# Kernel optimization log

Measured on AMD Instinct MI355X. Metric: run time of the kernel, lower is better.

The kernel has to match this reference:

```python
import jax, jax.numpy as jnp
import numpy as np
from jax import lax

DIM, HEADS, HIDDEN = 384, 6, 1536
B, D, H, W = 2, 14, 14, 14
LN_EPS = 1e-5


def setup_inputs() -> dict:
    key = jax.random.key(0)
    ks = jax.random.split(key, 8)
    s = 0.02
    return {
        "x": jax.random.normal(ks[0], (B, DIM, D, H, W), jnp.float32),
        "conv_w": jax.random.normal(ks[1], (DIM, 1, 3, 3, 3), jnp.float32) * s,
        "conv_b": jnp.zeros((DIM,), jnp.float32),
        "ln1_w": jnp.ones((DIM,), jnp.float32),
        "ln1_b": jnp.zeros((DIM,), jnp.float32),
        "qkv_w": jax.random.normal(ks[2], (3 * DIM, DIM), jnp.float32) * s,
        "proj_w": jax.random.normal(ks[3], (DIM, DIM), jnp.float32) * s,
        "proj_b": jnp.zeros((DIM,), jnp.float32),
        "ln2_w": jnp.ones((DIM,), jnp.float32),
        "ln2_b": jnp.zeros((DIM,), jnp.float32),
        "fc1_w": jax.random.normal(ks[4], (HIDDEN, DIM), jnp.float32) * s,
        "fc1_b": jnp.zeros((HIDDEN,), jnp.float32),
        "fc2_w": jax.random.normal(ks[5], (DIM, HIDDEN), jnp.float32) * s,
        "fc2_b": jnp.zeros((DIM,), jnp.float32),
    }


def _layernorm(x, w, b):
    mu = jnp.mean(x, axis=-1, keepdims=True)
    var = jnp.var(x, axis=-1, keepdims=True)
    return (x - mu) * lax.rsqrt(var + LN_EPS) * w + b


def reference(x, conv_w, conv_b, ln1_w, ln1_b, qkv_w, proj_w, proj_b,
              ln2_w, ln2_b, fc1_w, fc1_b, fc2_w, fc2_b):
    Bn, C = x.shape[0], x.shape[1]
    Dd, Hh, Ww = x.shape[2], x.shape[3], x.shape[4]
    # depthwise conv3d positional embedding (groups=dim), padding=1
    pos = lax.conv_general_dilated(
        x, conv_w, window_strides=(1, 1, 1), padding="SAME",
        feature_group_count=C,
        dimension_numbers=("NCDHW", "OIDHW", "NCDHW"))
    x = x + pos + conv_b[None, :, None, None, None] * 0 + conv_b[None, :, None, None, None]
    # fix: bias belongs to conv output only once
    x = x - conv_b[None, :, None, None, None]
    N = Dd * Hh * Ww
    t = x.reshape(Bn, C, N).transpose(0, 2, 1)  # [B, N, C]

    # attention
    hd = C // HEADS
    scale = hd ** -0.5
    tn = _layernorm(t, ln1_w, ln1_b)
    qkv = tn @ qkv_w.T  # [B, N, 3C]
    qkv = qkv.reshape(Bn, N, 3, HEADS, hd).transpose(2, 0, 3, 1, 4)
    q, k, v = qkv[0], qkv[1], qkv[2]  # [B, H, N, hd]
    attn = jax.nn.softmax(jnp.einsum("bhnd,bhmd->bhnm", q, k) * scale, axis=-1)
    o = jnp.einsum("bhnm,bhmd->bhnd", attn, v)
    o = o.transpose(0, 2, 1, 3).reshape(Bn, N, C)
    t = t + o @ proj_w.T + proj_b

    # MLP (exact GELU, matching torch nn.GELU default)
    tn2 = _layernorm(t, ln2_w, ln2_b)
    h = jax.nn.gelu(tn2 @ fc1_w.T + fc1_b, approximate=False)
    t = t + h @ fc2_w.T + fc2_b

    return t.transpose(0, 2, 1).reshape(Bn, C, Dd, Hh, Ww)
```

## Files before the change

### kernel.cpp

```cpp
#include <hip/hip_runtime.h>
#include <hip/hip_bf16.h>
#include <math.h>

#define DIM 384
#define HEADS 6
#define HIDDEN 1536
#define NTOK 2744
#define BATCH 2
#define MTOT (BATCH * NTOK)
#define KSPLIT 4
#define NQT 22
#define CEXP 0.18033688f

typedef __bf16 bf16x8 __attribute__((ext_vector_type(8)));
typedef __bf16 bf16x4 __attribute__((ext_vector_type(4)));
typedef float  f32x4  __attribute__((ext_vector_type(4)));

#define F_GELU  1
#define F_RESID 2
#define F_BF16  4
#define F_QKV   8
#define F_TRANS 16

__device__ __forceinline__ void gll16(const void* g, void* l) {
    __builtin_amdgcn_global_load_lds(
        (const __attribute__((address_space(1))) unsigned int*)g,
        (__attribute__((address_space(3))) unsigned int*)l, 16, 0, 0);
}

__global__ void k_conv(const float* __restrict__ x, const float* __restrict__ cw,
                       float* __restrict__ t,
                       const float* __restrict__ w0, const float* __restrict__ w1,
                       const float* __restrict__ w2, const float* __restrict__ w3,
                       __bf16* o0, __bf16* o1, __bf16* o2, __bf16* o3) {
    int bid = blockIdx.x;
    if (bid >= 528) {
        int i = (bid - 528) * 256 + threadIdx.x;
        const float* s; __bf16* d; int off;
        if (i < 110592)      { s = w0; d = o0; off = i; }
        else if (i < 147456) { s = w1; d = o1; off = i - 110592; }
        else if (i < 294912) { s = w2; d = o2; off = i - 147456; }
        else                 { s = w3; d = o3; off = i - 294912; }
        float4 v = ((const float4*)s)[off];
        bf16x4 bb = { (__bf16)v.x, (__bf16)v.y, (__bf16)v.z, (__bf16)v.w };
        *(bf16x4*)(d + (size_t)off * 4) = bb;
        return;
    }
    int nb = bid % 11, rest = bid / 11;
    int cb = rest % 24, b = rest / 24;
    int c0 = cb * 16;
    int n = nb * 256 + threadIdx.x;
    if (n >= NTOK) return;
    int d = n / 196, r = n % 196, h = r / 14, w = r % 14;
    const float* xb = x + ((size_t)b * DIM + c0) * NTOK;
    float acc[16];
    #pragma unroll
    for (int c = 0; c < 16; c++) acc[c] = xb[(size_t)c * NTOK + n];
    #pragma unroll
    for (int kd = 0; kd < 3; kd++) {
        int dd = d + kd - 1;
        if (dd < 0 || dd >= 14) continue;
        #pragma unroll
        for (int kh = 0; kh < 3; kh++) {
            int hh = h + kh - 1;
            if (hh < 0 || hh >= 14) continue;
            #pragma unroll
            for (int kw = 0; kw < 3; kw++) {
                int ww = w + kw - 1;
                if (ww < 0 || ww >= 14) continue;
                int np = (dd * 14 + hh) * 14 + ww;
                int tap = kd * 9 + kh * 3 + kw;
                #pragma unroll
                for (int c = 0; c < 16; c++)
                    acc[c] = fmaf(cw[(c0 + c) * 27 + tap], xb[(size_t)c * NTOK + np], acc[c]);
            }
        }
    }
    float* tp = t + (size_t)(b * NTOK + n) * DIM + c0;
    #pragma unroll
    for (int c = 0; c < 16; c += 4) {
        float4 v = { acc[c], acc[c + 1], acc[c + 2], acc[c + 3] };
        *(float4*)(tp + c) = v;
    }
}

__device__ __forceinline__ void ln_body(const float* __restrict__ in,
                                        __bf16* __restrict__ out,
                                        const float* __restrict__ w,
                                        const float* __restrict__ b) {
    int wid = threadIdx.x >> 6, lane = threadIdx.x & 63;
    int token = blockIdx.x * 4 + wid;
    const float* row = in + (size_t)token * DIM;
    float v[6], s = 0.f, s2 = 0.f;
    #pragma unroll
    for (int i = 0; i < 6; i++) {
        v[i] = row[lane + 64 * i];
        s += v[i]; s2 += v[i] * v[i];
    }
    #pragma unroll
    for (int m = 1; m < 64; m <<= 1) { s += __shfl_xor(s, m); s2 += __shfl_xor(s2, m); }
    float mu = s * (1.f / DIM);
    float rstd = rsqrtf(s2 * (1.f / DIM) - mu * mu + 1e-5f);
    __bf16* orow = out + (size_t)token * DIM;
    #pragma unroll
    for (int i = 0; i < 6; i++) {
        int c = lane + 64 * i;
        orow[c] = (__bf16)((v[i] - mu) * rstd * w[c] + b[c]);
    }
}
__global__ void k_ln1(const float* in, __bf16* out, const float* w, const float* b) {
    ln_body(in, out, w, b);
}
__global__ void k_ln2(const float* in, __bf16* out, const float* w, const float* b) {
    ln_body(in, out, w, b);
}

__device__ __forceinline__ void gemm12864_body(
    const __bf16* __restrict__ A, const __bf16* __restrict__ B,
    const float* __restrict__ bias, void* __restrict__ out,
    __bf16* __restrict__ vt_out, int M, int N, int K, int flags) {
    __shared__ __bf16 As[128][64];
    __shared__ __bf16 Bs[64][64];
    int tid = threadIdx.x, lane = tid & 63, wid = tid >> 6;
    int quad = lane >> 4, l16 = lane & 15;
    int wm = wid & 1, wn = wid >> 1;
    int m0 = blockIdx.y * 128, n0 = blockIdx.x * 64;
    int x7 = l16 & 7;

    auto stage = [&](int k0) {
        #pragma unroll
        for (int i = 0; i < 4; i++) {
            int c = i * 256 + tid;
            int row = c >> 3, cc = (c & 7) ^ (row & 7);
            int gm = m0 + row; if (gm > M - 1) gm = M - 1;
            gll16(A + (size_t)gm * K + k0 + cc * 8, &As[0][0] + (size_t)c * 8);
        }
        #pragma unroll
        for (int i = 0; i < 2; i++) {
            int c = i * 256 + tid;
            int row = c >> 3, cc = (c & 7) ^ (row & 7);
            gll16(B + (size_t)(n0 + row) * K + k0 + cc * 8, &Bs[0][0] + (size_t)c * 8);
        }
    };

    f32x4 acc[4][2] = {};
    int nk = K >> 6;
    for (int ki = 0; ki < nk; ki++) {
        if (ki) __syncthreads();
        stage(ki << 6);
        __syncthreads();
        #pragma unroll
        for (int s = 0; s < 2; s++) {
            bf16x8 a[4], b[2];
            #pragma unroll
            for (int i = 0; i < 4; i++)
                a[i] = *(bf16x8*)&As[wm * 64 + i * 16 + l16][(((s * 4 + quad) ^ x7)) * 8];
            #pragma unroll
            for (int j = 0; j < 2; j++)
                b[j] = *(bf16x8*)&Bs[wn * 32 + j * 16 + l16][(((s * 4 + quad) ^ x7)) * 8];
            #pragma unroll
            for (int i = 0; i < 4; i++)
                #pragma unroll
                for (int j = 0; j < 2; j++)
                    acc[i][j] = __builtin_amdgcn_mfma_f32_16x16x32_bf16(a[i], b[j], acc[i][j], 0, 0, 0);
        }
    }

    int colb = n0 + wn * 32;
    #pragma unroll
    for (int j = 0; j < 2; j++) {
        int col = colb + j * 16 + l16;
        float bv = bias ? bias[col] : 0.f;
        #pragma unroll
        for (int i = 0; i < 4; i++) {
            int row0 = m0 + wm * 64 + i * 16 + quad * 4;
            if (row0 >= M) continue;
            float v4[4];
            #pragma unroll
            for (int r = 0; r < 4; r++) {
                float v = acc[i][j][r] + bv;
                if (flags & F_GELU) v = 0.5f * v * (1.f + erff(v * 0.70710678f));
                if ((flags & F_QKV) && col < 384) v *= CEXP;
                v4[r] = v;
            }
            if ((flags & F_QKV) && col >= 768) {
                int b2 = row0 / NTOK, n2 = row0 - b2 * NTOK;
                bf16x4 pk = { (__bf16)v4[0], (__bf16)v4[1], (__bf16)v4[2], (__bf16)v4[3] };
                *(bf16x4*)(vt_out + ((size_t)(b2 * DIM + (col - 768))) * NTOK + n2) = pk;
            } else {
                #pragma unroll
                for (int r = 0; r < 4; r++)
                    ((__bf16*)out)[(size_t)(row0 + r) * N + col] = (__bf16)v4[r];
            }
        }
    }
}
__global__ __launch_bounds__(256) void k_qkv(const __bf16* A, const __bf16* B,
        void* out, __bf16* vt_out, int M, int N, int K) {
    gemm12864_body(A, B, nullptr, out, vt_out, M, N, K, F_QKV);
}
__global__ __launch_bounds__(256) void k_fc1(const __bf16* A, const __bf16* B,
        const float* bias, void* out, int M, int N, int K) {
    gemm12864_body(A, B, bias, out, nullptr, M, N, K, F_GELU | F_BF16);
}

__device__ __forceinline__ void gemm64_body(
    const __bf16* __restrict__ A, const __bf16* __restrict__ B,
    const float* __restrict__ bias, const float* __restrict__ resid,
    void* __restrict__ out, int M, int N, int K, int flags) {
    __shared__ __align__(16) char sm[17408];
    __bf16 (*As)[64] = (__bf16(*)[64])sm;
    __bf16 (*Bs)[64] = (__bf16(*)[64])(sm + 8192);
    float* Tt = (float*)sm;
    int tid = threadIdx.x, lane = tid & 63, wid = tid >> 6;
    int quad = lane >> 4, l16 = lane & 15;
    int wm = wid & 1, wn = wid >> 1;
    int m0 = blockIdx.y * 64, n0 = blockIdx.x * 64;
    int x7 = l16 & 7;

    auto stage = [&](int k0) {
        #pragma unroll
        for (int i = 0; i < 2; i++) {
            int c = i * 256 + tid;
            int row = c >> 3, cc = (c & 7) ^ (row & 7);
            int gm = m0 + row; if (gm > M - 1) gm = M - 1;
            gll16(A + (size_t)gm * K + k0 + cc * 8, &As[0][0] + (size_t)c * 8);
        }
        #pragma unroll
        for (int i = 0; i < 2; i++) {
            int c = i * 256 + tid;
            int row = c >> 3, cc = (c & 7) ^ (row & 7);
            gll16(B + (size_t)(n0 + row) * K + k0 + cc * 8, &Bs[0][0] + (size_t)c * 8);
        }
    };

    f32x4 acc[2][2] = {};
    int nk = K >> 6;
    for (int ki = 0; ki < nk; ki++) {
        if (ki) __syncthreads();
        stage(ki << 6);
        __syncthreads();
        #pragma unroll
        for (int s = 0; s < 2; s++) {
            bf16x8 a[2], b[2];
            #pragma unroll
            for (int i = 0; i < 2; i++)
                a[i] = *(bf16x8*)&As[wm * 32 + i * 16 + l16][(((s * 4 + quad) ^ x7)) * 8];
            #pragma unroll
            for (int j = 0; j < 2; j++)
                b[j] = *(bf16x8*)&Bs[wn * 32 + j * 16 + l16][(((s * 4 + quad) ^ x7)) * 8];
            #pragma unroll
            for (int i = 0; i < 2; i++)
                #pragma unroll
                for (int j = 0; j < 2; j++)
                    acc[i][j] = __builtin_amdgcn_mfma_f32_16x16x32_bf16(a[i], b[j], acc[i][j], 0, 0, 0);
        }
    }

    if (flags & F_TRANS) {
        #pragma unroll
        for (int half = 0; half < 2; half++) {
            __syncthreads();
            if (wn == half) {
                #pragma unroll
                for (int j = 0; j < 2; j++) {
                    int colL = j * 16 + l16;
                    int col = n0 + half * 32 + colL;
                    float bv = bias[col];
                    #pragma unroll
                    for (int i = 0; i < 2; i++) {
                        int rowL = wm * 32 + i * 16 + quad * 4;
                        float v4[4];
                        #pragma unroll
                        for (int r = 0; r < 4; r++) {
                            int rr = m0 + rowL + r; if (rr > M - 1) rr = M - 1;
                            v4[r] = acc[i][j][r] + bv + resid[(size_t)rr * N + col];
                        }
                        float4 pk = { v4[0], v4[1], v4[2], v4[3] };
                        *(float4*)&Tt[colL * 68 + rowL] = pk;
                    }
                }
            }
            __syncthreads();
            int c = tid >> 3, no = (tid & 7) * 8;
            int col = n0 + half * 32 + c;
            #pragma unroll
            for (int q2 = 0; q2 < 2; q2++) {
                int nn = no + q2 * 4;
                int row = m0 + nn;
                if (row >= M) continue;
                int b2 = row / NTOK, n2 = row - b2 * NTOK;
                float4 v = *(float4*)&Tt[c * 68 + nn];
                *(float4*)((float*)out + ((size_t)(b2 * N + col)) * NTOK + n2) = v;
            }
        }
        return;
    }

    #pragma unroll
    for (int j = 0; j < 2; j++) {
        int col = n0 + wn * 32 + j * 16 + l16;
        float bv = bias ? bias[col] : 0.f;
        #pragma unroll
        for (int i = 0; i < 2; i++) {
            int row0 = m0 + wm * 32 + i * 16 + quad * 4;
            if (row0 >= M) continue;
            #pragma unroll
            for (int r = 0; r < 4; r++) {
                float v = acc[i][j][r] + bv;
                if (flags & F_RESID) v += resid[(size_t)(row0 + r) * N + col];
                ((float*)out)[(size_t)(row0 + r) * N + col] = v;
            }
        }
    }
}
__global__ __launch_bounds__(256) void k_proj(const __bf16* A, const __bf16* B,
        const float* bias, const float* resid, void* out, int M, int N, int K) {
    gemm64_body(A, B, bias, resid, out, M, N, K, F_RESID);
}
__global__ __launch_bounds__(256) void k_fc2(const __bf16* A, const __bf16* B,
        const float* bias, const float* resid, void* out, int M, int N, int K) {
    gemm64_body(A, B, bias, resid, out, M, N, K, F_RESID | F_TRANS);
}

__global__ __launch_bounds__(256) void k_attn(const __bf16* __restrict__ qkv,
                                              const __bf16* __restrict__ vt,
                                              __bf16* __restrict__ opart,
                                              float* __restrict__ lpart) {
    __shared__ __align__(16) char smemQP[128 * 72 * 2];
    __shared__ __bf16 Ks[64][64];
    __shared__ __bf16 Vt[64][64];
    __bf16 (*Qs)[64] = (__bf16(*)[64])smemQP;
    __bf16 (*Ps)[72] = (__bf16(*)[72])smemQP;

    int tid = threadIdx.x, lane = tid & 63, wid = tid >> 6;
    int quad = lane >> 4, l16 = lane & 15;
    int q0 = blockIdx.x * 128;
    int bh = blockIdx.y;
    int ks = blockIdx.z;
    int b = bh / HEADS, h = bh % HEADS;
    int x7 = l16 & 7;

    auto stageKV = [&](int k0) {
        #pragma unroll
        for (int i = 0; i < 2; i++) {
            int c = i * 256 + tid;
            int row = c >> 3, cc = (c & 7) ^ (row & 7);
            int gk = k0 + row; if (gk > NTOK - 1) gk = NTOK - 1;
            gll16(qkv + ((size_t)(b * NTOK + gk)) * 1152 + 384 + h * 64 + cc * 8,
                  &Ks[0][0] + (size_t)c * 8);
            gll16(vt + ((size_t)(bh * 64 + row)) * NTOK + k0 + cc * 8,
                  &Vt[0][0] + (size_t)c * 8);
        }
    };

    int kt0 = (43 * ks) / KSPLIT, kt1 = (43 * (ks + 1)) / KSPLIT;

    #pragma unroll
    for (int i = 0; i < 4; i++) {
        int c = i * 256 + tid;
        int row = c >> 3, cc = (c & 7) ^ (row & 7);
        int gq = q0 + row; if (gq > NTOK - 1) gq = NTOK - 1;
        gll16(qkv + ((size_t)(b * NTOK + gq)) * 1152 + h * 64 + cc * 8,
              &Qs[0][0] + (size_t)c * 8);
    }
    stageKV(kt0 * 64);
    __syncthreads();

    bf16x8 aq[2][2];
    #pragma unroll
    for (int qt = 0; qt < 2; qt++)
        #pragma unroll
        for (int s = 0; s < 2; s++)
            aq[qt][s] = *(bf16x8*)&Qs[wid * 32 + qt * 16 + l16][((s * 4 + quad) ^ x7) * 8];
    __syncthreads();

    f32x4 oacc[2][4] = {};
    float l_part[2][4] = {};
    __bf16* pwr = &Ps[wid * 32 + quad * 4][l16];
    const __bf16* prd = &Ps[wid * 32 + l16][0];

    for (int kt = kt0; kt < kt1; kt++) {
        if (kt > kt0) {
            __syncthreads();
            stageKV(kt * 64);
            __syncthreads();
        }
        int k0 = kt * 64;

        f32x4 s[2][4];
        #pragma unroll
        for (int t = 0; t < 4; t++) {
            bf16x8 bk0 = *(bf16x8*)&Ks[t * 16 + l16][((quad) ^ x7) * 8];
            bf16x8 bk1 = *(bf16x8*)&Ks[t * 16 + l16][((4 + quad) ^ x7) * 8];
            #pragma unroll
            for (int qt = 0; qt < 2; qt++) {
                f32x4 z = {0.f, 0.f, 0.f, 0.f};
                z = __builtin_amdgcn_mfma_f32_16x16x32_bf16(aq[qt][0], bk0, z, 0, 0, 0);
                s[qt][t] = __builtin_amdgcn_mfma_f32_16x16x32_bf16(aq[qt][1], bk1, z, 0, 0, 0);
            }
        }
        if (k0 + 64 > NTOK) {
            #pragma unroll
            for (int t = 0; t < 4; t++)
                if (k0 + t * 16 + l16 >= NTOK)
                    #pragma unroll
                    for (int qt = 0; qt < 2; qt++) {
                        s[qt][t][0] = -1e30f; s[qt][t][1] = -1e30f;
                        s[qt][t][2] = -1e30f; s[qt][t][3] = -1e30f;
                    }
        }
        #pragma unroll
        for (int qt = 0; qt < 2; qt++)
            #pragma unroll
            for (int t = 0; t < 4; t++)
                #pragma unroll
                for (int r = 0; r < 4; r++) {
                    float e = exp2f(s[qt][t][r]);
                    l_part[qt][r] += e;
                    pwr[(qt * 16 + r) * 72 + t * 16] = (__bf16)e;
                }
        bf16x8 ap[2][2];
        #pragma unroll
        for (int qt = 0; qt < 2; qt++)
            #pragma unroll
            for (int sx = 0; sx < 2; sx++)
                ap[qt][sx] = *(bf16x8*)(prd + qt * 16 * 72 + sx * 32 + quad * 8);
        #pragma unroll
        for (int t = 0; t < 4; t++) {
            bf16x8 bv0 = *(bf16x8*)&Vt[t * 16 + l16][((quad) ^ x7) * 8];
            bf16x8 bv1 = *(bf16x8*)&Vt[t * 16 + l16][((4 + quad) ^ x7) * 8];
            #pragma unroll
            for (int qt = 0; qt < 2; qt++) {
                oacc[qt][t] = __builtin_amdgcn_mfma_f32_16x16x32_bf16(ap[qt][0], bv0, oacc[qt][t], 0, 0, 0);
                oacc[qt][t] = __builtin_amdgcn_mfma_f32_16x16x32_bf16(ap[qt][1], bv1, oacc[qt][t], 0, 0, 0);
            }
        }
    }

    #pragma unroll
    for (int qt = 0; qt < 2; qt++)
        #pragma unroll
        for (int r = 0; r < 4; r++) {
            int gq = q0 + wid * 32 + qt * 16 + quad * 4 + r;
            if (gq >= NTOK) continue;
            float l = l_part[qt][r];
            #pragma unroll
            for (int mk = 1; mk < 16; mk <<= 1) l += __shfl_xor(l, mk);
            if (l16 == 0) lpart[((size_t)ks * 12 + bh) * NTOK + gq] = l;
            __bf16* op = opart + ((size_t)ks * MTOT + (size_t)b * NTOK + gq) * DIM + h * 64;
            #pragma unroll
            for (int t = 0; t < 4; t++) op[t * 16 + l16] = (__bf16)oacc[qt][t][r];
        }
}

__global__ void k_comb(const __bf16* __restrict__ opart,
                       const float* __restrict__ lpart,
                       __bf16* __restrict__ o) {
    int idx = blockIdx.x * 256 + threadIdx.x;
    int token = idx / 96, rem = idx - token * 96;
    int c = rem * 4, h = c >> 6;
    int b2 = token / NTOK, n = token - b2 * NTOK;
    int bh = b2 * HEADS + h;
    float a0 = 0.f, a1 = 0.f, a2 = 0.f, a3 = 0.f, l = 0.f;
    #pragma unroll
    for (int ks = 0; ks < KSPLIT; ks++) {
        bf16x4 p = *(const bf16x4*)&opart[((size_t)ks * MTOT + token) * DIM + c];
        a0 += (float)p[0]; a1 += (float)p[1]; a2 += (float)p[2]; a3 += (float)p[3];
        l += lpart[((size_t)ks * 12 + bh) * NTOK + n];
    }
    float inv = 1.f / l;
    bf16x4 ov = { (__bf16)(a0 * inv), (__bf16)(a1 * inv),
                  (__bf16)(a2 * inv), (__bf16)(a3 * inv) };
    *(bf16x4*)(o + (size_t)token * DIM + c) = ov;
}

extern "C" void kernel_launch(void* const* d_in, const int* in_sizes, int n_in,
                              void* d_out, int out_size, void* d_ws, size_t ws_size,
                              hipStream_t stream) {
    const float* x      = (const float*)d_in[0];
    const float* conv_w = (const float*)d_in[1];
    const float* ln1_w  = (const float*)d_in[3];
    const float* ln1_b  = (const float*)d_in[4];
    const float* qkv_w  = (const float*)d_in[5];
    const float* proj_w = (const float*)d_in[6];
    const float* proj_b = (const float*)d_in[7];
    const float* ln2_w  = (const float*)d_in[8];
    const float* ln2_b  = (const float*)d_in[9];
    const float* fc1_w  = (const float*)d_in[10];
    const float* fc1_b  = (const float*)d_in[11];
    const float* fc2_w  = (const float*)d_in[12];
    const float* fc2_b  = (const float*)d_in[13];
    float* out = (float*)d_out;

    char* p = (char*)d_ws;
    float*  T    = (float*)p;  p += (size_t)MTOT * DIM * 4;
    __bf16* TN   = (__bf16*)p; p += (size_t)MTOT * DIM * 2;
    __bf16* QKV  = (__bf16*)p; p += (size_t)MTOT * 1152 * 2;
    __bf16* VT   = (__bf16*)p; p += (size_t)BATCH * DIM * NTOK * 2;
    __bf16* O    = (__bf16*)p; p += (size_t)MTOT * DIM * 2;
    __bf16* H    = (__bf16*)p; p += (size_t)MTOT * HIDDEN * 2;
    __bf16* WQ   = (__bf16*)p; p += (size_t)1152 * 384 * 2;
    __bf16* WP   = (__bf16*)p; p += (size_t)384 * 384 * 2;
    __bf16* W1   = (__bf16*)p; p += (size_t)1536 * 384 * 2;
    __bf16* W2   = (__bf16*)p; p += (size_t)384 * 1536 * 2;
    float*  LP   = (float*)p;  p += (size_t)KSPLIT * 12 * NTOK * 4;
    __bf16* OP   = (__bf16*)p; p += (size_t)KSPLIT * MTOT * DIM * 2;

    k_conv<<<528 + 1728, 256, 0, stream>>>(
        x, conv_w, T, qkv_w, proj_w, fc1_w, fc2_w, WQ, WP, W1, W2);
    k_ln1<<<MTOT / 4, 256, 0, stream>>>(T, TN, ln1_w, ln1_b);
    k_qkv<<<dim3(18, 43), 256, 0, stream>>>(TN, WQ, QKV, VT, MTOT, 1152, 384);
    k_attn<<<dim3(NQT, 12, KSPLIT), 256, 0, stream>>>(QKV, VT, OP, LP);
    k_comb<<<(MTOT * 96) / 256, 256, 0, stream>>>(OP, LP, O);
    k_proj<<<dim3(6, 86), 256, 0, stream>>>(O, WP, proj_b, T, T, MTOT, 384, 384);
    k_ln2<<<MTOT / 4, 256, 0, stream>>>(T, TN, ln2_w, ln2_b);
    k_fc1<<<dim3(24, 43), 256, 0, stream>>>(TN, W1, fc1_b, H, MTOT, 1536, 384);
    k_fc2<<<dim3(6, 86), 256, 0, stream>>>(H, W2, fc2_b, T, out, MTOT, 384, 1536);
}
```

Measured before the change: 232.2 us.

## Double-buffer K/V in attention, widen blocks to 512 threads, transpose S MFMA

The attention kernel now uses 512-thread blocks covering 256 queries each, so every K/V tile staged in LDS is reused by twice as many query rows. K/V staging is double-buffered, so the next tile's global-to-LDS load overlaps with compute on the current one and one barrier per iteration is removed. The score MFMA operands are swapped so each lane holds four consecutive keys of one query. That lets exp, the tail masking and the row sum run in registers, with packed bf16x4 writes of P into a swizzled LDS layout and a shorter shuffle reduction for the row sums. In exchange the grid has half as many blocks and each block uses more LDS, which may lower occupancy.

```diff
diff --git a/kernel.cpp b/kernel.cpp
--- a/kernel.cpp
+++ b/kernel.cpp
@@ -9,7 +9,7 @@
 #define BATCH 2
 #define MTOT (BATCH * NTOK)
 #define KSPLIT 4
-#define NQT 22
+#define NQT 11
 #define CEXP 0.18033688f
 
 typedef __bf16 bf16x8 __attribute__((ext_vector_type(8)));
@@ -323,48 +323,47 @@
     gemm64_body(A, B, bias, resid, out, M, N, K, F_RESID | F_TRANS);
 }
 
-__global__ __launch_bounds__(256) void k_attn(const __bf16* __restrict__ qkv,
-                                              const __bf16* __restrict__ vt,
-                                              __bf16* __restrict__ opart,
-                                              float* __restrict__ lpart) {
-    __shared__ __align__(16) char smemQP[128 * 72 * 2];
-    __shared__ __bf16 Ks[64][64];
-    __shared__ __bf16 Vt[64][64];
+__global__ __launch_bounds__(512, 4) void k_attn(const __bf16* __restrict__ qkv,
+                                                 const __bf16* __restrict__ vt,
+                                                 __bf16* __restrict__ opart,
+                                                 float* __restrict__ lpart) {
+    __shared__ __align__(16) char smemQP[256 * 64 * 2];
+    __shared__ __align__(16) __bf16 Ks[2][64][64];
+    __shared__ __align__(16) __bf16 Vt[2][64][64];
     __bf16 (*Qs)[64] = (__bf16(*)[64])smemQP;
-    __bf16 (*Ps)[72] = (__bf16(*)[72])smemQP;
+    __bf16* PB = (__bf16*)smemQP;
 
     int tid = threadIdx.x, lane = tid & 63, wid = tid >> 6;
     int quad = lane >> 4, l16 = lane & 15;
-    int q0 = blockIdx.x * 128;
+    int q0 = blockIdx.x * 256;
     int bh = blockIdx.y;
     int ks = blockIdx.z;
     int b = bh / HEADS, h = bh % HEADS;
     int x7 = l16 & 7;
 
-    auto stageKV = [&](int k0) {
-        #pragma unroll
-        for (int i = 0; i < 2; i++) {
-            int c = i * 256 + tid;
-            int row = c >> 3, cc = (c & 7) ^ (row & 7);
-            int gk = k0 + row; if (gk > NTOK - 1) gk = NTOK - 1;
-            gll16(qkv + ((size_t)(b * NTOK + gk)) * 1152 + 384 + h * 64 + cc * 8,
-                  &Ks[0][0] + (size_t)c * 8);
-            gll16(vt + ((size_t)(bh * 64 + row)) * NTOK + k0 + cc * 8,
-                  &Vt[0][0] + (size_t)c * 8);
-        }
+    int kt0 = (43 * ks) / KSPLIT, kt1 = (43 * (ks + 1)) / KSPLIT;
+
+    int srow = tid >> 3, scc = (tid & 7) ^ (srow & 7);
+    const __bf16* pK = qkv + ((size_t)(b * NTOK + kt0 * 64 + srow)) * 1152 + 384 + h * 64 + scc * 8;
+    const __bf16* pV = vt + ((size_t)(bh * 64 + srow)) * NTOK + kt0 * 64 + scc * 8;
+
+    auto stageKV = [&](int kt, int bufi) {
+        const __bf16* kp = pK + (size_t)(kt - kt0) * (64 * 1152);
+        if (kt == 42 && srow >= 56)
+            kp = qkv + ((size_t)(b * NTOK + NTOK - 1)) * 1152 + 384 + h * 64 + scc * 8;
+        gll16(kp, &Ks[bufi][0][0] + (size_t)tid * 8);
+        gll16(pV + (size_t)(kt - kt0) * 64, &Vt[bufi][0][0] + (size_t)tid * 8);
     };
 
-    int kt0 = (43 * ks) / KSPLIT, kt1 = (43 * (ks + 1)) / KSPLIT;
-
     #pragma unroll
     for (int i = 0; i < 4; i++) {
-        int c = i * 256 + tid;
+        int c = i * 512 + tid;
         int row = c >> 3, cc = (c & 7) ^ (row & 7);
         int gq = q0 + row; if (gq > NTOK - 1) gq = NTOK - 1;
         gll16(qkv + ((size_t)(b * NTOK + gq)) * 1152 + h * 64 + cc * 8,
               &Qs[0][0] + (size_t)c * 8);
     }
-    stageKV(kt0 * 64);
+    stageKV(kt0, 0);
     __syncthreads();
 
     bf16x8 aq[2][2];
@@ -375,67 +374,79 @@
             aq[qt][s] = *(bf16x8*)&Qs[wid * 32 + qt * 16 + l16][((s * 4 + quad) ^ x7) * 8];
     __syncthreads();
 
+    unsigned pso[4], pro[2];
+    #pragma unroll
+    for (int t = 0; t < 4; t++)
+        pso[t] = (unsigned)(wid * 32 + l16) * 64
+               + ((unsigned)((t * 2 + (quad >> 1)) ^ x7) * 8 + (quad & 1) * 4);
+    #pragma unroll
+    for (int sx = 0; sx < 2; sx++)
+        pro[sx] = (unsigned)(wid * 32 + l16) * 64
+                + (unsigned)(((sx * 4 + quad) ^ x7) * 8);
+
+    const f32x4 fzero = {0.f, 0.f, 0.f, 0.f};
     f32x4 oacc[2][4] = {};
-    float l_part[2][4] = {};
-    __bf16* pwr = &Ps[wid * 32 + quad * 4][l16];
-    const __bf16* prd = &Ps[wid * 32 + l16][0];
-
+    float l_lane[2] = {0.f, 0.f};
+
+    int bufi = 0;
     for (int kt = kt0; kt < kt1; kt++) {
-        if (kt > kt0) {
-            __syncthreads();
-            stageKV(kt * 64);
-            __syncthreads();
-        }
-        int k0 = kt * 64;
-
-        f32x4 s[2][4];
+        if (kt > kt0) __syncthreads();
+        if (kt + 1 < kt1) stageKV(kt + 1, bufi ^ 1);
+
+        const __bf16* ksb = &Ks[bufi][0][0] + l16 * 64;
+        const __bf16* vtb = &Vt[bufi][0][0] + l16 * 64;
+        bool tail = (kt == 42);
+
         #pragma unroll
         for (int t = 0; t < 4; t++) {
-            bf16x8 bk0 = *(bf16x8*)&Ks[t * 16 + l16][((quad) ^ x7) * 8];
-            bf16x8 bk1 = *(bf16x8*)&Ks[t * 16 + l16][((4 + quad) ^ x7) * 8];
+            bf16x8 bk0 = *(bf16x8*)(ksb + t * 1024 + ((quad ^ x7) * 8));
+            bf16x8 bk1 = *(bf16x8*)(ksb + t * 1024 + (((4 + quad) ^ x7) * 8));
             #pragma unroll
             for (int qt = 0; qt < 2; qt++) {
-                f32x4 z = {0.f, 0.f, 0.f, 0.f};
-                z = __builtin_amdgcn_mfma_f32_16x16x32_bf16(aq[qt][0], bk0, z, 0, 0, 0);
-                s[qt][t] = __builtin_amdgcn_mfma_f32_16x16x32_bf16(aq[qt][1], bk1, z, 0, 0, 0);
-            }
-        }
-        if (k0 + 64 > NTOK) {
-            #pragma unroll
-            for (int t = 0; t < 4; t++)
-                if (k0 + t * 16 + l16 >= NTOK)
-                    #pragma unroll
-                    for (int qt = 0; qt < 2; qt++) {
-                        s[qt][t][0] = -1e30f; s[qt][t][1] = -1e30f;
-                        s[qt][t][2] = -1e30f; s[qt][t][3] = -1e30f;
-                    }
-        }
+                f32x4 z = __builtin_amdgcn_mfma_f32_16x16x32_bf16(bk0, aq[qt][0], fzero, 0, 0, 0);
+                z = __builtin_amdgcn_mfma_f32_16x16x32_bf16(bk1, aq[qt][1], z, 0, 0, 0);
+                float e0 = exp2f(z[0]), e1 = exp2f(z[1]), e2 = exp2f(z[2]), e3 = exp2f(z[3]);
+                if (tail) {
+                    int kb = kt * 64 + t * 16 + quad * 4;
+                    if (kb + 0 >= NTOK) e0 = 0.f;
+                    if (kb + 1 >= NTOK) e1 = 0.f;
+                    if (kb + 2 >= NTOK) e2 = 0.f;
+                    if (kb + 3 >= NTOK) e3 = 0.f;
+                }
+                l_lane[qt] += (e0 + e1) + (e2 + e3);
+                bf16x4 pk = { (__bf16)e0, (__bf16)e1, (__bf16)e2, (__bf16)e3 };
+                *(bf16x4*)(PB + pso[t] + qt * 1024) = pk;
+            }
+        }
+
+        bf16x8 ap[2][2];
         #pragma unroll
         for (int qt = 0; qt < 2; qt++)
             #pragma unroll
-            for (int t = 0; t < 4; t++)
-                #pragma unroll
-                for (int r = 0; r < 4; r++) {
-                    float e = exp2f(s[qt][t][r]);
-                    l_part[qt][r] += e;
-                    pwr[(qt * 16 + r) * 72 + t * 16] = (__bf16)e;
-                }
-        bf16x8 ap[2][2];
-        #pragma unroll
-        for (int qt = 0; qt < 2; qt++)
-            #pragma unroll
             for (int sx = 0; sx < 2; sx++)
-                ap[qt][sx] = *(bf16x8*)(prd + qt * 16 * 72 + sx * 32 + quad * 8);
+                ap[qt][sx] = *(bf16x8*)(PB + pro[sx] + qt * 1024);
+
         #pragma unroll
         for (int t = 0; t < 4; t++) {
-            bf16x8 bv0 = *(bf16x8*)&Vt[t * 16 + l16][((quad) ^ x7) * 8];
-            bf16x8 bv1 = *(bf16x8*)&Vt[t * 16 + l16][((4 + quad) ^ x7) * 8];
+            bf16x8 bv0 = *(bf16x8*)(vtb + t * 1024 + ((quad ^ x7) * 8));
+            bf16x8 bv1 = *(bf16x8*)(vtb + t * 1024 + (((4 + quad) ^ x7) * 8));
             #pragma unroll
             for (int qt = 0; qt < 2; qt++) {
                 oacc[qt][t] = __builtin_amdgcn_mfma_f32_16x16x32_bf16(ap[qt][0], bv0, oacc[qt][t], 0, 0, 0);
                 oacc[qt][t] = __builtin_amdgcn_mfma_f32_16x16x32_bf16(ap[qt][1], bv1, oacc[qt][t], 0, 0, 0);
             }
         }
+        bufi ^= 1;
+    }
+
+    #pragma unroll
+    for (int qt = 0; qt < 2; qt++) {
+        float l = l_lane[qt];
+        l += __shfl_xor(l, 16);
+        l += __shfl_xor(l, 32);
+        int gq = q0 + wid * 32 + qt * 16 + l16;
+        if (quad == 0 && gq < NTOK)
+            lpart[((size_t)ks * 12 + bh) * NTOK + gq] = l;
     }
 
     #pragma unroll
@@ -444,10 +455,6 @@
         for (int r = 0; r < 4; r++) {
             int gq = q0 + wid * 32 + qt * 16 + quad * 4 + r;
             if (gq >= NTOK) continue;
-            float l = l_part[qt][r];
-            #pragma unroll
-            for (int mk = 1; mk < 16; mk <<= 1) l += __shfl_xor(l, mk);
-            if (l16 == 0) lpart[((size_t)ks * 12 + bh) * NTOK + gq] = l;
             __bf16* op = opart + ((size_t)ks * MTOT + (size_t)b * NTOK + gq) * DIM + h * 64;
             #pragma unroll
             for (int t = 0; t < 4; t++) op[t * 16 + l16] = (__bf16)oacc[qt][t][r];
@@ -511,7 +518,7 @@
         x, conv_w, T, qkv_w, proj_w, fc1_w, fc2_w, WQ, WP, W1, W2);
     k_ln1<<<MTOT / 4, 256, 0, stream>>>(T, TN, ln1_w, ln1_b);
     k_qkv<<<dim3(18, 43), 256, 0, stream>>>(TN, WQ, QKV, VT, MTOT, 1152, 384);
-    k_attn<<<dim3(NQT, 12, KSPLIT), 256, 0, stream>>>(QKV, VT, OP, LP);
+    k_attn<<<dim3(NQT, 12, KSPLIT), 512, 0, stream>>>(QKV, VT, OP, LP);
     k_comb<<<(MTOT * 96) / 256, 256, 0, stream>>>(OP, LP, O);
     k_proj<<<dim3(6, 86), 256, 0, stream>>>(O, WP, proj_b, T, T, MTOT, 384, 384);
     k_ln2<<<MTOT / 4, 256, 0, stream>>>(T, TN, ln2_w, ln2_b);
```

After: 232.7 us. About the same (+0.2%).
